# Optimization experiments

Measured on AMD Instinct MI355X. Metric: run time of the kernel, lower is better.

The kernel has to match this reference:

```python
import jax, jax.numpy as jnp
import numpy as np

B, C, H = 2, 32, 64  # batch, base channel, bottleneck spatial size
EPS = 1e-5


def _conv(x, w, b, pad):
    # standard NCHW conv, stride 1
    out = jax.lax.conv_general_dilated(x, w, (1, 1), [(pad, pad), (pad, pad)],
                                       dimension_numbers=("NCHW", "OIHW", "NCHW"))
    return out + b[None, :, None, None]


def _inorm(x):
    # InstanceNorm2d, affine=False (torch default)
    m = jnp.mean(x, axis=(2, 3), keepdims=True)
    v = jnp.var(x, axis=(2, 3), keepdims=True)
    return (x - m) * jax.lax.rsqrt(v + EPS)


def _patches3(x):
    # x: (B,C,H,W) -> (B,C,9,H-2,W-2); 3x3 patches, stride 1, VALID
    oh, ow = x.shape[-2] - 2, x.shape[-1] - 2
    return jnp.stack([x[:, :, i:i + oh, j:j + ow] for i in range(3) for j in range(3)], axis=2)


def _pac_kernel(g):
    # gaussian pixel-adaptive kernel (NVlabs/pac, kernel_type='gaussian', normalize_kernel=False)
    # g: (B,Cg,H,W) -> K: (B,9,H,W), K = exp(-0.5*||f_nbr - f_center||^2)
    gp = jnp.pad(g, ((0, 0), (0, 0), (1, 1), (1, 1)))
    p = _patches3(gp)                      # (B,Cg,9,H,W)
    d = p - g[:, :, None]                  # center is offset (1,1) == g itself
    return jnp.exp(-0.5 * jnp.sum(d * d, axis=1))


def _pacconvT(x, g, w, b):
    # PacConvTranspose2d: kernel_size=3, stride=2, padding=1, output_padding=1
    # native impl: zero-upsample, pad (k-1)-p=1 left/top and 1+out_pad=2 right/bottom,
    # then pixel-adaptive conv with weight.permute(1,0,2,3) (no spatial flip, per PAC).
    Bc, Cin, Hh, Ww = x.shape
    z = jnp.zeros((Bc, Cin, 2 * Hh - 1, 2 * Ww - 1), x.dtype).at[:, :, ::2, ::2].set(x)
    z = jnp.pad(z, ((0, 0), (0, 0), (1, 2), (1, 2)))
    p = _patches3(z)                       # (B,Cin,9,2H,2W)
    k = _pac_kernel(g)                     # (B,9,2H,2W)
    wf = jnp.transpose(w, (1, 0, 2, 3)).reshape(w.shape[1], w.shape[0], 9)  # (Cout,Cin,9)
    out = jnp.einsum('bckhw,bkhw,ock->bohw', p, k, wf)
    return out + b[None, :, None, None]


def _w(key, shape, scale):
    return jax.random.normal(key, shape, dtype=jnp.float32) * scale


def setup_inputs():
    key = jax.random.key(0)
    ks = jax.random.split(key, 20)
    return {
        "x": jax.random.normal(ks[0], (B, 8 * C, H, H), jnp.float32),
        "ef_lv2": jax.random.normal(ks[1], (B, 2 * C, 2 * H, 2 * H), jnp.float32),
        "ef_lv1": jax.random.normal(ks[2], (B, C, 4 * H, 4 * H), jnp.float32),
        "W_down": _w(ks[3], (4 * C, 8 * C, 3, 3), (8 * C * 9) ** -0.5),
        "b_down": _w(ks[4], (4 * C,), 0.01),
        "W_mid": _w(ks[5], (4 * C, 4 * C, 1, 1), (4 * C) ** -0.5),
        "b_mid": _w(ks[6], (4 * C,), 0.01),
        "W_adj2": _w(ks[7], (4 * C, 2 * C, 3, 3), 0.002),  # small: keeps gaussian kernel non-degenerate
        "b_adj2": _w(ks[8], (4 * C,), 0.01),
        "W_adj1": _w(ks[9], (2 * C, C, 3, 3), 0.004),
        "b_adj1": _w(ks[10], (2 * C,), 0.01),
        "W16": _w(ks[11], (4 * C, 2 * C, 3, 3), (4 * C * 9) ** -0.5),  # convT layout (Cin,Cout,kh,kw)
        "b16": _w(ks[12], (2 * C,), 0.01),
        "W20": _w(ks[13], (2 * C, C, 3, 3), (2 * C * 9) ** -0.5),
        "b20": _w(ks[14], (C,), 0.01),
        "W24": _w(ks[15], (3, C, 3, 3), (C * 9) ** -0.5),
        "b24": _w(ks[16], (3,), 0.01),
    }


def reference(x, ef_lv2, ef_lv1, W_down, b_down, W_mid, b_mid, W_adj2, b_adj2,
              W_adj1, b_adj1, W16, b16, W20, b20, W24, b24):
    x = _conv(_inorm(x), W_down, b_down, 1)          # layer13: norm + channel-down 8C->4C
    x = _conv(x, W_mid, b_mid, 0) + x                # middle_layer13 1x1 + residual
    g2 = _conv(ef_lv2, W_adj2, b_adj2, 1)            # adjust_ef_lv2 2C->4C
    x = _pacconvT(x, g2, W16, b16)                   # layer16: 4C->2C, x2 spatial
    x = _inorm(x) + x                                # layer17 + residual (twice)
    x = _inorm(x) + x
    g1 = _conv(ef_lv1, W_adj1, b_adj1, 1)            # adjust_ef_lv1 C->2C
    x = _pacconvT(x, g1, W20, b20)                   # layer20: 2C->C, x2 spatial
    x = _inorm(x) + x                                # layer21 + residual (twice)
    x = _inorm(x) + x
    return _conv(x, W24, b24, 1)                     # layer24: C->3
```

## Files before the change

### kernel.cpp

```cpp
#include <hip/hip_runtime.h>

#define EPS 1e-5f

typedef short sh8 __attribute__((ext_vector_type(8)));
typedef float f32x4 __attribute__((ext_vector_type(4)));

__device__ __forceinline__ ushort f2b(float f) {
    unsigned u = __float_as_uint(f);
    u += 0x7fffu + ((u >> 16) & 1u);
    return (ushort)(u >> 16);
}

__device__ __forceinline__ void istat_body(int ch, const float* __restrict__ in,
                                           float* st, int HW)
{
    __shared__ double sh[512];
    const float* p = in + (size_t)ch * HW;
    double s = 0.0, s2 = 0.0;
    for (int i = threadIdx.x * 4; i < HW; i += 1024) {
        float4 v = *(const float4*)(p + i);
        s  += (double)v.x + (double)v.y + (double)v.z + (double)v.w;
        s2 += (double)v.x * v.x + (double)v.y * v.y
            + (double)v.z * v.z + (double)v.w * v.w;
    }
    sh[threadIdx.x] = s; sh[256 + threadIdx.x] = s2;
    __syncthreads();
    for (int o = 128; o > 0; o >>= 1) {
        if ((int)threadIdx.x < o) {
            sh[threadIdx.x]       += sh[threadIdx.x + o];
            sh[256 + threadIdx.x] += sh[256 + threadIdx.x + o];
        }
        __syncthreads();
    }
    if (threadIdx.x == 0) {
        double m = sh[0] / (double)HW;
        double v = sh[256] / (double)HW - m * m;
        st[2 * ch]     = (float)m;
        st[2 * ch + 1] = (float)(v < 0.0 ? 0.0 : v);
    }
}

__device__ __forceinline__ void ipad_body(int bxi, int b,
    const float* __restrict__ in, const float* __restrict__ st,
    ushort* __restrict__ ob, int C, int H, int W, int pad, int n4)
{
    int idx = bxi * 256 + threadIdx.x;
    if (idx >= n4) return;
    int cpp = C >> 2;
    int pp = idx / cpp, c0 = (idx - pp * cpp) * 4;
    int Wp = W + 2 * pad, Hp = H + 2 * pad;
    int yp = pp / Wp, xp = pp - yp * Wp;
    int y = yp - pad, x = xp - pad;
    ushort4 o;
    if (y >= 0 && y < H && x >= 0 && x < W) {
        size_t HW = (size_t)H * W;
        const float* ib = in + (size_t)b * C * HW + (size_t)y * W + x;
        #pragma unroll
        for (int u = 0; u < 4; u++) {
            int chg = b * C + c0 + u;
            float m = st[2 * chg];
            float inv = rsqrtf(st[2 * chg + 1] + EPS);
            float v = ib[(size_t)(c0 + u) * HW];
            ((ushort*)&o)[u] = f2b((v - m) * inv);
        }
    } else { o.x = o.y = o.z = o.w = 0; }
    *(ushort4*)(ob + ((size_t)b * Hp * Wp + pp) * C + c0) = o;
}

__device__ __forceinline__ void pad_body(int bxi, int b,
    const float* __restrict__ in, ushort* __restrict__ ob,
    int C, int H, int W, int pad, int n4)
{
    int idx = bxi * 256 + threadIdx.x;
    if (idx >= n4) return;
    int cpp = C >> 2;
    int pp = idx / cpp, c0 = (idx - pp * cpp) * 4;
    int Wp = W + 2 * pad, Hp = H + 2 * pad;
    int yp = pp / Wp, xp = pp - yp * Wp;
    int y = yp - pad, x = xp - pad;
    ushort4 o;
    if (y >= 0 && y < H && x >= 0 && x < W) {
        const float* ib = in + ((size_t)b * C) * H * W + (size_t)y * W + x;
        size_t HW = (size_t)H * W;
        o.x = f2b(ib[(size_t)(c0    ) * HW]);
        o.y = f2b(ib[(size_t)(c0 + 1) * HW]);
        o.z = f2b(ib[(size_t)(c0 + 2) * HW]);
        o.w = f2b(ib[(size_t)(c0 + 3) * HW]);
    } else { o.x = o.y = o.z = o.w = 0; }
    *(ushort4*)(ob + ((size_t)b * Hp * Wp + pp) * C + c0) = o;
}

__device__ __forceinline__ void wprep_body(int bxi,
    const float* W16, const float* W20, const float* Wd, const float* Wa2,
    const float* Wa1,
    ushort* wT1b, ushort* wT2b, ushort* wbD, ushort* wbA2b, ushort* wbA1b)
{
    int idx = bxi * 256 + threadIdx.x;
    if (idx < 73728) {
        int to = idx / 128, ci = idx - to * 128;
        int t = to / 64, o = to - t * 64;
        wT1b[idx] = f2b(W16[((size_t)ci * 64 + o) * 9 + t]);
        return;
    } idx -= 73728;
    if (idx < 18432) {
        int to = idx / 64, ci = idx - to * 64;
        int t = to / 32, o = to - t * 32;
        wT2b[idx] = f2b(W20[((size_t)ci * 32 + o) * 9 + t]);
        return;
    } idx -= 18432;
    if (idx < 294912) {
        int co = idx / 2304, r = idx - co * 2304;
        int t = r / 256, ci = r - t * 256;
        wbD[idx] = f2b(Wd[((size_t)co * 256 + ci) * 9 + t]);
        return;
    } idx -= 294912;
    if (idx < 73728) {
        int co = idx / 576, r = idx - co * 576;
        int t = r / 64, ci = r - t * 64;
        wbA2b[idx] = f2b(Wa2[((size_t)co * 64 + ci) * 9 + t]);
        return;
    } idx -= 73728;
    if (idx < 18432) {
        int co = idx / 288, r = idx - co * 288;
        int t = r / 32, ci = r - t * 32;
        wbA1b[idx] = f2b(Wa1[((size_t)co * 32 + ci) * 9 + t]);
        return;
    }
}

template<int CI, int TAPS, int KCH, int CPB>
__device__ __forceinline__ void mg2f_body(int bx, int by, int b,
    const ushort* __restrict__ inb, const ushort* __restrict__ wb,
    const float* __restrict__ bias, float* __restrict__ outp,
    int wshift, int Wp, size_t in_bstride, size_t out_bstride, int HW,
    ushort* bsm)
{
    constexpr int CPBSH = (CPB == 1) ? 0 : (CPB == 2) ? 1 : 2;
    constexpr int SPR   = TAPS * CPB;
    constexpr int TOT   = TAPS * KCH;
    constexpr int PS    = SPR * 32 + 8;

    int tid = threadIdx.x;
    int wv = tid >> 6, l = tid & 63;
    int lane16 = l & 15, quad = l >> 4;
    int klane = quad * 8;
    int pb = bx * 128 + wv * 32;
    int nb0 = by * 32;

    int base[2];
    #pragma unroll
    for (int i = 0; i < 2; i++) {
        int pm = pb + i * 16 + lane16;
        if (TAPS == 9) {
            int W = 1 << wshift;
            int y = pm >> wshift, xx = pm & (W - 1);
            base[i] = (y + 1) * Wp + (xx + 1);
        } else base[i] = pm;
    }
    int nn[2];
    nn[0] = nb0 + lane16; nn[1] = nb0 + 16 + lane16;

    const ushort* inbb = inb + (size_t)b * in_bstride + klane;
    const ushort* bp0 = bsm + lane16 * PS + klane;
    const ushort* bp1 = bsm + (16 + lane16) * PS + klane;

    f32x4 vz = {0.f, 0.f, 0.f, 0.f};
    f32x4 acc[2][2] = {{vz, vz}, {vz, vz}};
    sh8 A[3][2];

    #define LDA(ss, av) { \
        int r_ = (ss) / SPR; int l_ = (ss) - r_ * SPR; \
        int t_ = l_ >> CPBSH; int ch_ = r_ * CPB + (l_ & (CPB - 1)); \
        int dof_ = 0; \
        if (TAPS == 9) { \
            int dy_ = (t_ * 43) >> 7; \
            int dx_ = t_ - dy_ * 3; \
            dof_ = (dy_ - 1) * Wp + (dx_ - 1); \
        } \
        av[0] = *(const sh8*)(inbb + (size_t)(base[0] + dof_) * CI + (ch_ << 5)); \
        av[1] = *(const sh8*)(inbb + (size_t)(base[1] + dof_) * CI + (ch_ << 5)); \
    }

    LDA(0, A[0])
    if (TOT > 1) LDA(1, A[1])

    #pragma unroll
    for (int r = 0; r < KCH / CPB; r++) {
        if (r) __syncthreads();
        {
            constexpr int elems = 32 * SPR * 4;
            for (int j = tid; j < elems; j += 256) {
                int n  = j / (SPR * 4);
                int rr = j - n * (SPR * 4);
                int kc = rr >> 2, c8 = rr & 3;
                int t_ = kc >> CPBSH, co = kc & (CPB - 1);
                int ch_ = r * CPB + co;
                sh8 v = *(const sh8*)(wb
                    + ((size_t)(nb0 + n) * TAPS + t_) * CI + (ch_ << 5) + (c8 << 3));
                *(sh8*)(bsm + n * PS + (kc << 5) + (c8 << 3)) = v;
            }
        }
        __syncthreads();
        #pragma unroll
        for (int li = 0; li < SPR; li++) {
            const int s = r * SPR + li;
            if (s + 2 < TOT) LDA(s + 2, A[(s + 2) % 3])
            sh8 b0 = *(const sh8*)(bp0 + (li << 5));
            sh8 b1 = *(const sh8*)(bp1 + (li << 5));
            acc[0][0] = __builtin_amdgcn_mfma_f32_16x16x32_bf16(A[s % 3][0], b0, acc[0][0], 0, 0, 0);
            acc[0][1] = __builtin_amdgcn_mfma_f32_16x16x32_bf16(A[s % 3][0], b1, acc[0][1], 0, 0, 0);
            acc[1][0] = __builtin_amdgcn_mfma_f32_16x16x32_bf16(A[s % 3][1], b0, acc[1][0], 0, 0, 0);
            acc[1][1] = __builtin_amdgcn_mfma_f32_16x16x32_bf16(A[s % 3][1], b1, acc[1][1], 0, 0, 0);
        }
    }
    #undef LDA

    float* ob = outp + (size_t)b * out_bstride;
    #pragma unroll
    for (int j = 0; j < 2; j++) {
        float bb = bias ? bias[nn[j]] : 0.f;
        #pragma unroll
        for (int i = 0; i < 2; i++) {
            int p0 = pb + i * 16 + quad * 4;
            *(float4*)(ob + (size_t)nn[j] * HW + p0) =
                make_float4(acc[i][j][0] + bb, acc[i][j][1] + bb,
                            acc[i][j][2] + bb, acc[i][j][3] + bb);
        }
    }
}

__device__ __forceinline__ void pack4_body(int bxi, int zy,
    const float* __restrict__ g, float* __restrict__ part,
    int Cg, int CS, int H, int W, int NS, size_t SS)
{
    int b = zy / NS, sl = zy - b * NS;
    int WC = W >> 2;
    int idx = bxi * 256 + threadIdx.x;
    int y = idx / WC, xc = idx - y * WC;
    int x0 = xc << 2;
    bool lz = (x0 == 0), rz = (x0 + 4 == W);
    float acc[9][4];
    #pragma unroll
    for (int t = 0; t < 9; t++)
        #pragma unroll
        for (int p = 0; p < 4; p++) acc[t][p] = 0.f;

    const float* gb = g + ((size_t)b * Cg + sl * CS) * H * W;
    for (int ci = 0; ci < CS; ci++) {
        const float* gc = gb + (size_t)ci * H * W;
        float e[3][6];
        #pragma unroll
        for (int r = 0; r < 3; r++) {
            int yy = y + r - 1;
            float4 v = make_float4(0.f, 0.f, 0.f, 0.f);
            if (yy >= 0 && yy < H)
                v = *(const float4*)(gc + (size_t)yy * W + x0);
            float lf = __shfl_up(v.w, 1);
            float rt = __shfl_down(v.x, 1);
            e[r][0] = lz ? 0.f : lf;
            e[r][1] = v.x; e[r][2] = v.y; e[r][3] = v.z; e[r][4] = v.w;
            e[r][5] = rz ? 0.f : rt;
        }
        #pragma unroll
        for (int i = 0; i < 3; i++)
            #pragma unroll
            for (int j = 0; j < 3; j++)
                #pragma unroll
                for (int p = 0; p < 4; p++) {
                    float d = e[i][p + j] - e[1][p + 1];
                    acc[i * 3 + j][p] = fmaf(d, d, acc[i * 3 + j][p]);
                }
    }
    size_t HW = (size_t)H * W;
    #pragma unroll
    for (int t = 0; t < 9; t++) {
        float4 o;
        if (NS == 1) {
            o = make_float4(expf(-0.5f * acc[t][0]), expf(-0.5f * acc[t][1]),
                            expf(-0.5f * acc[t][2]), expf(-0.5f * acc[t][3]));
        } else {
            o = make_float4(acc[t][0], acc[t][1], acc[t][2], acc[t][3]);
        }
        *(float4*)(part + (size_t)sl * SS + ((size_t)b * 9 + t) * HW
                   + (size_t)y * W + x0) = o;
    }
}

__device__ __forceinline__ void reduce_body(int bxi,
    const float* __restrict__ part, const float* __restrict__ bias,
    const float* res, float* out, int HW, int Co, int NS, size_t SS)
{
    int i4 = (bxi * 256 + threadIdx.x) * 4;
    float4 a = make_float4(0.f, 0.f, 0.f, 0.f);
    for (int s = 0; s < NS; s++) {
        float4 p = *(const float4*)(part + (size_t)s * SS + i4);
        a.x += p.x; a.y += p.y; a.z += p.z; a.w += p.w;
    }
    int c = (i4 / HW) % Co;
    float bb = bias[c];
    if (res) {
        float4 r = *(const float4*)(res + i4);
        a.x += r.x; a.y += r.y; a.z += r.z; a.w += r.w;
    }
    *(float4*)(out + i4) = make_float4(a.x + bb, a.y + bb, a.z + bb, a.w + bb);
}

__device__ __forceinline__ void expcomb_body(int bxi,
    const float* __restrict__ part, float* __restrict__ K, int NS, size_t SS)
{
    int i4 = (bxi * 256 + threadIdx.x) * 4;
    float4 a = make_float4(0.f, 0.f, 0.f, 0.f);
    for (int s = 0; s < NS; s++) {
        float4 p = *(const float4*)(part + (size_t)s * SS + i4);
        a.x += p.x; a.y += p.y; a.z += p.z; a.w += p.w;
    }
    *(float4*)(K + i4) = make_float4(expf(-0.5f * a.x), expf(-0.5f * a.y),
                                     expf(-0.5f * a.z), expf(-0.5f * a.w));
}

template<int NCO>
__device__ __forceinline__ void conv1x1_body(int bx, int by, int bz,
    const float* __restrict__ in, const float* __restrict__ w,
    float* __restrict__ outp, int C, int CS, int HW, int NS, size_t SS)
{
    int b = bz / NS, sl = bz - b * NS;
    int x0 = (bx * 256 + threadIdx.x) * 4;
    int co0 = by * NCO;
    float acc[NCO][4];
    #pragma unroll
    for (int j = 0; j < NCO; j++)
        #pragma unroll
        for (int p = 0; p < 4; p++) acc[j][p] = 0.f;
    const float* ib = in + ((size_t)b * C + sl * CS) * HW;
    for (int ci = 0; ci < CS; ci++) {
        float4 v = *(const float4*)(ib + (size_t)ci * HW + x0);
        int cig = sl * CS + ci;
        #pragma unroll
        for (int j = 0; j < NCO; j++) {
            float wv = w[(size_t)(co0 + j) * C + cig];
            acc[j][0] = fmaf(v.x, wv, acc[j][0]);
            acc[j][1] = fmaf(v.y, wv, acc[j][1]);
            acc[j][2] = fmaf(v.z, wv, acc[j][2]);
            acc[j][3] = fmaf(v.w, wv, acc[j][3]);
        }
    }
    #pragma unroll
    for (int j = 0; j < NCO; j++) {
        float* op = outp + (size_t)sl * SS + ((size_t)b * C + co0 + j) * HW + x0;
        *(float4*)op = make_float4(acc[j][0], acc[j][1], acc[j][2], acc[j][3]);
    }
}

__global__ __launch_bounds__(256) void pro_k(
    const float* x, const float* ef2, const float* ef1,
    const float* W16, const float* W20, const float* Wd, const float* Wa2,
    const float* Wa1,
    ushort* wT1b, ushort* wT2b, ushort* wbD, ushort* wbA2b, ushort* wbA1b,
    float* st0, ushort* padA2b, ushort* padA1b)
{
    int bid = blockIdx.x;
    if (bid < 1872) {
        wprep_body(bid, W16, W20, Wd, Wa2, Wa1, wT1b, wT2b, wbD, wbA2b, wbA1b);
        return;
    } bid -= 1872;
    if (bid < 512) { istat_body(bid, x, st0, 4096); return; } bid -= 512;
    if (bid < 2114) {
        pad_body(bid % 1057, bid / 1057, ef2, padA2b, 64, 128, 128, 1, 270400);
        return;
    } bid -= 2114;
    pad_body(bid % 2081, bid / 2081, ef1, padA1b, 32, 256, 256, 1, 532512);
}

__global__ __launch_bounds__(256) void l1_k(
    const float* x, const float* st0, ushort* padDb,
    const ushort* padA2b, const ushort* wbA2b, const float* ba2, float* g2,
    const ushort* padA1b, const ushort* wbA1b, const float* ba1, float* g1)
{
    __shared__ ushort smem[32 * (9 * 32 + 8)];
    int bid = blockIdx.x;
    if (bid < 2178) {
        ipad_body(bid % 1089, bid / 1089, x, st0, padDb, 256, 64, 64, 1, 278784);
        return;
    } bid -= 2178;
    if (bid < 1024) {
        mg2f_body<64, 9, 2, 1>(bid & 127, (bid >> 7) & 3, bid >> 9,
            padA2b, wbA2b, ba2, g2, 7, 130,
            (size_t)1081600, (size_t)2097152, 16384, smem);
        return;
    } bid -= 1024;
    mg2f_body<32, 9, 1, 1>(bid & 511, (bid >> 9) & 1, bid >> 10,
        padA1b, wbA1b, ba1, g1, 8, 258,
        (size_t)2130048, (size_t)4194304, 65536, smem);
}

__global__ __launch_bounds__(256) void l2_k(
    const ushort* padDb, const ushort* wbD, const float* bd, float* x1,
    const float* g1, float* K1, const float* g2, float* PK2)
{
    __shared__ ushort smem[32 * (9 * 32 + 8)];
    int bid = blockIdx.x;
    if (bid < 256) {
        mg2f_body<256, 9, 8, 1>(bid & 31, (bid >> 5) & 3, bid >> 7,
            padDb, wbD, bd, x1, 6, 66,
            (size_t)1115136, (size_t)524288, 4096, smem);
        return;
    } bid -= 256;
    if (bid < 128) {
        pack4_body(bid & 63, bid >> 6, g1, K1, 64, 64, 256, 256, 1, (size_t)0);
        return;
    } bid -= 128;
    pack4_body(bid & 15, bid >> 4, g2, PK2, 128, 64, 128, 128, 2, (size_t)294912);
}

__global__ __launch_bounds__(256) void l3_k(
    const float* x1, const float* Wm, float* Pm,
    const float* PK2, float* K2)
{
    int bid = blockIdx.x;
    if (bid < 512) {
        conv1x1_body<8>(bid & 3, (bid >> 2) & 15, bid >> 6,
                        x1, Wm, Pm, 128, 32, 4096, 4, (size_t)1048576);
        return;
    }
    expcomb_body(bid - 512, PK2, K2, 2, (size_t)294912);
}

__global__ __launch_bounds__(256) void istat1_k(const float* __restrict__ in,
                                                float* st, int HW)
{
    istat_body(blockIdx.x, in, st, HW);
}

template<int CI, int TAPS, int KCH, int CPB>
__global__ __launch_bounds__(256) void mg2f_k(
    const ushort* __restrict__ inb, const ushort* __restrict__ wb,
    const float* __restrict__ bias, float* __restrict__ outp,
    int wshift, int Wp, size_t in_bstride, size_t out_bstride, int HW)
{
    constexpr int PS = TAPS * CPB * 32 + 8;
    __shared__ ushort smem[32 * PS];
    mg2f_body<CI, TAPS, KCH, CPB>(blockIdx.x, blockIdx.y, blockIdx.z,
        inb, wb, bias, outp, wshift, Wp, in_bstride, out_bstride, HW, smem);
}

__global__ __launch_bounds__(256) void iapad_k(const float* __restrict__ in,
    const float* __restrict__ st, ushort* __restrict__ ob, int HW, int Co)
{
    int i4 = (blockIdx.x * 256 + threadIdx.x) * 4;
    int ch = i4 / HW;
    int p = i4 - ch * HW;
    int b = ch / Co, c = ch - b * Co;
    float m = st[2 * ch];
    float inv = rsqrtf(st[2 * ch + 1] + EPS);
    float4 v = *(const float4*)(in + i4);
    ushort* op = ob + ((size_t)b * HW + p) * Co + c;
    op[0]              = f2b(v.x + 2.f * (v.x - m) * inv);
    op[(size_t)Co]     = f2b(v.y + 2.f * (v.y - m) * inv);
    op[(size_t)Co * 2] = f2b(v.z + 2.f * (v.z - m) * inv);
    op[(size_t)Co * 3] = f2b(v.w + 2.f * (v.w - m) * inv);
}

template<int NCO>
__global__ __launch_bounds__(256) void conv3x3_d(const float* __restrict__ in,
    const float* __restrict__ w, const float* __restrict__ bias,
    float* __restrict__ outp, const float* __restrict__ st,
    int Ci, int CS, int H, int W, int Co, int NS, size_t SS)
{
    int z = blockIdx.z;
    int b = z / NS, sl = z - b * NS;
    int WC = W >> 2;
    int idx = blockIdx.x * 256 + threadIdx.x;
    int xc = idx % WC, y = idx / WC;
    int x0 = xc << 2;
    bool lz = (x0 == 0), rz = (x0 + 4 == W);
    int co0 = blockIdx.y * NCO;
    float acc[NCO][4];
    #pragma unroll
    for (int j = 0; j < NCO; j++)
        #pragma unroll
        for (int p = 0; p < 4; p++) acc[j][p] = 0.f;

    const float* ib = in + ((size_t)b * Ci + sl * CS) * H * W;
    for (int ci = 0; ci < CS; ci++) {
        const float* ic = ib + (size_t)ci * H * W;
        int cig = sl * CS + ci;
        float sa = 1.f, sb = 0.f;
        if (st) {
            int chg = b * Ci + cig;
            float m = st[2 * chg];
            float inv = rsqrtf(st[2 * chg + 1] + EPS);
            sa = 1.f + 2.f * inv;
            sb = -2.f * m * inv;
        }
        float e[3][6];
        #pragma unroll
        for (int r = 0; r < 3; r++) {
            int yy = y + r - 1;
            float4 v = make_float4(0.f, 0.f, 0.f, 0.f);
            if (yy >= 0 && yy < H) {
                v = *(const float4*)(ic + (size_t)yy * W + x0);
                if (st) {
                    v.x = fmaf(v.x, sa, sb); v.y = fmaf(v.y, sa, sb);
                    v.z = fmaf(v.z, sa, sb); v.w = fmaf(v.w, sa, sb);
                }
            }
            float lf = __shfl_up(v.w, 1);
            float rt = __shfl_down(v.x, 1);
            e[r][0] = lz ? 0.f : lf;
            e[r][1] = v.x; e[r][2] = v.y; e[r][3] = v.z; e[r][4] = v.w;
            e[r][5] = rz ? 0.f : rt;
        }
        #pragma unroll
        for (int j = 0; j < NCO; j++) {
            const float* wj = w + ((size_t)(co0 + j) * Ci + cig) * 9;
            #pragma unroll
            for (int r = 0; r < 3; r++) {
                float w0 = wj[3 * r], w1 = wj[3 * r + 1], w2 = wj[3 * r + 2];
                #pragma unroll
                for (int p = 0; p < 4; p++)
                    acc[j][p] = fmaf(e[r][p], w0,
                                fmaf(e[r][p + 1], w1,
                                fmaf(e[r][p + 2], w2, acc[j][p])));
            }
        }
    }
    size_t HW = (size_t)H * W;
    #pragma unroll
    for (int j = 0; j < NCO; j++) {
        float bb = bias ? bias[co0 + j] : 0.f;
        float4 o = make_float4(acc[j][0] + bb, acc[j][1] + bb,
                               acc[j][2] + bb, acc[j][3] + bb);
        float* op = outp + (size_t)sl * SS
                  + ((size_t)b * Co + co0 + j) * HW + (size_t)y * W + x0;
        *(float4*)op = o;
    }
}

__global__ __launch_bounds__(256) void reduce_k(const float* __restrict__ part,
    const float* __restrict__ bias, const float* res, float* out,
    int HW, int Co, int NS, size_t SS)
{
    reduce_body(blockIdx.x, part, bias, res, out, HW, Co, NS, SS);
}

__global__ __launch_bounds__(256) void reduceb_k(const float* __restrict__ part,
    const float* __restrict__ bias, const float* __restrict__ res,
    ushort* __restrict__ ob, int HW, int Co, int NS, size_t SS)
{
    int i4 = (blockIdx.x * 256 + threadIdx.x) * 4;
    int ch = i4 / HW;
    int p = i4 - ch * HW;
    int b = ch / Co, c = ch - b * Co;
    float4 a = make_float4(0.f, 0.f, 0.f, 0.f);
    for (int s = 0; s < NS; s++) {
        float4 pv = *(const float4*)(part + (size_t)s * SS + i4);
        a.x += pv.x; a.y += pv.y; a.z += pv.z; a.w += pv.w;
    }
    float bb = bias[c];
    float4 r = *(const float4*)(res + i4);
    a.x += r.x + bb; a.y += r.y + bb; a.z += r.z + bb; a.w += r.w + bb;
    ushort* op = ob + ((size_t)b * HW + p) * Co + c;
    op[0]              = f2b(a.x);
    op[(size_t)Co]     = f2b(a.y);
    op[(size_t)Co * 2] = f2b(a.z);
    op[(size_t)Co * 3] = f2b(a.w);
}

template<int NCO>
__global__ __launch_bounds__(256) void pacsc_k(const float* __restrict__ Gin,
    const float* __restrict__ K, const float* __restrict__ bias,
    float* __restrict__ out, int Cout, int Hi, int Wi, size_t gstride)
{
    int b = blockIdx.z;
    int H = Hi << 1, W = Wi << 1;
    int HW = H * W, HWi = Hi * Wi, WC = W >> 2;
    int idx = blockIdx.x * 256 + threadIdx.x;
    int half = (H >> 1) * WC;
    int py = (idx >= half) ? 1 : 0;
    int r = idx - py * half;
    int ry = r / WC;
    int y = 2 * ry + py;
    int x0 = (r - ry * WC) << 2;
    int yi = y >> 1, xi0 = x0 >> 1;
    int co0 = blockIdx.y * NCO;
    const float* G  = Gin + (size_t)b * gstride;
    const float* Kb = K + (size_t)b * 9 * HW;
    float* ob = out + (size_t)b * Cout * HW;
    size_t krow = (size_t)y * W + x0;
    bool vok = (xi0 + 2 < Wi);

    if (py == 0) {
        float k4a = Kb[(size_t)4 * HW + krow],     k4b = Kb[(size_t)4 * HW + krow + 2];
        float k3a = Kb[(size_t)3 * HW + krow + 1], k3b = Kb[(size_t)3 * HW + krow + 3];
        float k5a = Kb[(size_t)5 * HW + krow + 1], k5b = Kb[(size_t)5 * HW + krow + 3];
        #pragma unroll
        for (int j = 0; j < NCO; j++) {
            int co = co0 + j;
            size_t rowb = (size_t)yi * Wi + xi0;
            const float* g3 = G + (size_t)(3 * Cout + co) * HWi + rowb;
            const float* g4 = G + (size_t)(4 * Cout + co) * HWi + rowb;
            const float* g5 = G + (size_t)(5 * Cout + co) * HWi + rowb;
            float bb = bias[co];
            float g5b = vok ? g5[2] : 0.f;
            float o0 = fmaf(k4a, g4[0], bb);
            float o1 = fmaf(k3a, g3[0], fmaf(k5a, g5[1], bb));
            float o2 = fmaf(k4b, g4[1], bb);
            float o3 = fmaf(k3b, g3[1], fmaf(k5b, g5b, bb));
            *(float4*)(ob + (size_t)co * HW + krow) = make_float4(o0, o1, o2, o3);
        }
    } else {
        bool yok = (yi + 1 < Hi);
        float k1a = Kb[(size_t)1 * HW + krow],     k1b = Kb[(size_t)1 * HW + krow + 2];
        float k7a = Kb[(size_t)7 * HW + krow],     k7b = Kb[(size_t)7 * HW + krow + 2];
        float k0a = Kb[(size_t)0 * HW + krow + 1], k0b = Kb[(size_t)0 * HW + krow + 3];
        float k2a = Kb[(size_t)2 * HW + krow + 1], k2b = Kb[(size_t)2 * HW + krow + 3];
        float k6a = Kb[(size_t)6 * HW + krow + 1], k6b = Kb[(size_t)6 * HW + krow + 3];
        float k8a = Kb[(size_t)8 * HW + krow + 1], k8b = Kb[(size_t)8 * HW + krow + 3];
        #pragma unroll
        for (int j = 0; j < NCO; j++) {
            int co = co0 + j;
            size_t row0 = (size_t)yi * Wi + xi0;
            size_t row1 = (size_t)(yi + 1) * Wi + xi0;
            const float* g0 = G + (size_t)(0 * Cout + co) * HWi + row0;
            const float* g1 = G + (size_t)(1 * Cout + co) * HWi + row0;
            const float* g2 = G + (size_t)(2 * Cout + co) * HWi + row0;
            const float* g6 = G + (size_t)(6 * Cout + co) * HWi + row1;
            const float* g7 = G + (size_t)(7 * Cout + co) * HWi + row1;
            const float* g8 = G + (size_t)(8 * Cout + co) * HWi + row1;
            float bb = bias[co];
            float g2b = vok ? g2[2] : 0.f;
            float g6a = yok ? g6[0] : 0.f, g6b = yok ? g6[1] : 0.f;
            float g7a = yok ? g7[0] : 0.f, g7b = yok ? g7[1] : 0.f;
            float g8a = yok ? g8[1] : 0.f;
            float g8b = (yok && vok) ? g8[2] : 0.f;
            float o0 = fmaf(k1a, g1[0], fmaf(k7a, g7a, bb));
            float o1 = fmaf(k0a, g0[0], fmaf(k2a, g2[1],
                       fmaf(k6a, g6a, fmaf(k8a, g8a, bb))));
            float o2 = fmaf(k1b, g1[1], fmaf(k7b, g7b, bb));
            float o3 = fmaf(k0b, g0[1], fmaf(k2b, g2b,
                       fmaf(k6b, g6b, fmaf(k8b, g8b, bb))));
            *(float4*)(ob + (size_t)co * HW + krow) = make_float4(o0, o1, o2, o3);
        }
    }
}

extern "C" void kernel_launch(void* const* d_in, const int* in_sizes, int n_in,
                              void* d_out, int out_size, void* d_ws, size_t ws_size,
                              hipStream_t stream)
{
    const float* x   = (const float*)d_in[0];
    const float* ef2 = (const float*)d_in[1];
    const float* ef1 = (const float*)d_in[2];
    const float* Wd  = (const float*)d_in[3];
    const float* bd  = (const float*)d_in[4];
    const float* Wm  = (const float*)d_in[5];
    const float* bm  = (const float*)d_in[6];
    const float* Wa2 = (const float*)d_in[7];
    const float* ba2 = (const float*)d_in[8];
    const float* Wa1 = (const float*)d_in[9];
    const float* ba1 = (const float*)d_in[10];
    const float* W16 = (const float*)d_in[11];
    const float* b16 = (const float*)d_in[12];
    const float* W20 = (const float*)d_in[13];
    const float* b20 = (const float*)d_in[14];
    const float* W24 = (const float*)d_in[15];
    const float* b24 = (const float*)d_in[16];
    float* out = (float*)d_out;

    float* P = (float*)d_ws;
    size_t o = 0;
    auto take = [&](size_t n) { float* p = P + o; o += n; return p; };
    ushort* padDb  = (ushort*)take(1115136);
    ushort* wbD    = (ushort*)take(147456);
    float*  x1     = take(1048576);
    float*  Pm     = take(4194304);
    ushort* x2b    = (ushort*)take(524288);
    ushort* padA2b = (ushort*)take(1081600);
    ushort* wbA2b  = (ushort*)take(36864);
    float*  g2     = take(4194304);
    float*  PK2    = take(589824);
    float*  K2     = take(294912);
    float*  Gin1   = take(4718592);
    float*  x3     = take(2097152);
    ushort* x3b    = (ushort*)take(1048576);
    ushort* padA1b = (ushort*)take(2130048);
    ushort* wbA1b  = (ushort*)take(9216);
    float*  g1     = take(4194304);
    float*  K1     = take(1179648);
    float*  Gin2   = take(9437184);
    float*  x5     = take(4194304);
    float*  Pf     = take(1572864);
    ushort* wT1b   = (ushort*)take(36864);
    ushort* wT2b   = (ushort*)take(9216);
    float*  ST     = take(1408);
    float* st0 = ST; float* st3 = ST + 1024; float* st5 = ST + 1280;

    pro_k<<<dim3(8660), dim3(256), 0, stream>>>(
        x, ef2, ef1, W16, W20, Wd, Wa2, Wa1,
        wT1b, wT2b, wbD, wbA2b, wbA1b, st0, padA2b, padA1b);

    l1_k<<<dim3(5250), dim3(256), 0, stream>>>(
        x, st0, padDb, padA2b, wbA2b, ba2, g2, padA1b, wbA1b, ba1, g1);

    l2_k<<<dim3(448), dim3(256), 0, stream>>>(
        padDb, wbD, bd, x1, g1, K1, g2, PK2);

    l3_k<<<dim3(800), dim3(256), 0, stream>>>(x1, Wm, Pm, PK2, K2);

    reduceb_k<<<dim3(1024), dim3(256), 0, stream>>>(Pm, bm, x1, x2b, 4096, 128, 4, 1048576);

    mg2f_k<128, 1, 4, 4><<<dim3(32, 18, 2), dim3(256), 0, stream>>>(
        x2b, wT1b, nullptr, Gin1, 0, 0,
        (size_t)524288, (size_t)2359296, 4096);
    pacsc_k<2><<<dim3(16, 32, 2), dim3(256), 0, stream>>>(
        Gin1, K2, b16, x3, 64, 64, 64, (size_t)2359296);

    istat1_k<<<dim3(128), dim3(256), 0, stream>>>(x3, st3, 16384);
    iapad_k<<<dim3(2048), dim3(256), 0, stream>>>(x3, st3, x3b, 16384, 64);

    mg2f_k<64, 1, 2, 2><<<dim3(128, 9, 2), dim3(256), 0, stream>>>(
        x3b, wT2b, nullptr, Gin2, 0, 0,
        (size_t)1048576, (size_t)4718592, 16384);
    pacsc_k<2><<<dim3(64, 16, 2), dim3(256), 0, stream>>>(
        Gin2, K1, b20, x5, 32, 128, 128, (size_t)4718592);

    istat1_k<<<dim3(64), dim3(256), 0, stream>>>(x5, st5, 65536);

    conv3x3_d<3><<<dim3(64, 1, 8), dim3(256), 0, stream>>>(
        x5, W24, nullptr, Pf, st5, 32, 8, 256, 256, 3, 4, (size_t)393216);
    reduce_k<<<dim3(384), dim3(256), 0, stream>>>(Pf, b24, nullptr, out, 65536, 3, 4, 393216);
}
```

Before: 370.0 us.

## Split-K the down conv across 8 slices and fuse 1x1 conv with residual

The 3x3 channel-down MFMA conv (256 input channels) is split into 8 input-channel slices, each writing partial sums. A reduce then adds bias to form x1, raising the block count from 256 to 2048 for better occupancy. The 1x1 middle conv now runs in one kernel with weights in shared memory and fuses bias, residual and the bf16 channel-last packing, replacing the separate split conv plus reduceb pass. The g2 pack step also computes K2 in a single slice, which drops the expcomb step. The cost is a larger partial buffer and extra memory traffic for the split-K reduction.

```diff
diff --git a/kernel.cpp b/kernel.cpp
--- a/kernel.cpp
+++ b/kernel.cpp
@@ -129,17 +129,19 @@
 }
 
 template<int CI, int TAPS, int KCH, int CPB>
-__device__ __forceinline__ void mg2f_body(int bx, int by, int b,
+__device__ __forceinline__ void mg2f_body(int bx, int by, int bz,
     const ushort* __restrict__ inb, const ushort* __restrict__ wb,
     const float* __restrict__ bias, float* __restrict__ outp,
-    int wshift, int Wp, size_t in_bstride, size_t out_bstride, int HW,
-    ushort* bsm)
+    int wshift, int Wp, int NS, size_t SS,
+    size_t in_bstride, size_t out_bstride, int HW, ushort* bsm)
 {
     constexpr int CPBSH = (CPB == 1) ? 0 : (CPB == 2) ? 1 : 2;
     constexpr int SPR   = TAPS * CPB;
     constexpr int TOT   = TAPS * KCH;
     constexpr int PS    = SPR * 32 + 8;
 
+    int b = bz / NS, sl = bz - b * NS;
+    int cilo = sl * (KCH * 32);
     int tid = threadIdx.x;
     int wv = tid >> 6, l = tid & 63;
     int lane16 = l & 15, quad = l >> 4;
@@ -160,7 +162,8 @@
     int nn[2];
     nn[0] = nb0 + lane16; nn[1] = nb0 + 16 + lane16;
 
-    const ushort* inbb = inb + (size_t)b * in_bstride + klane;
+    const ushort* inbb = inb + (size_t)b * in_bstride + cilo + klane;
+    const ushort* wbs  = wb + cilo;
     const ushort* bp0 = bsm + lane16 * PS + klane;
     const ushort* bp1 = bsm + (16 + lane16) * PS + klane;
 
@@ -195,7 +198,7 @@
                 int kc = rr >> 2, c8 = rr & 3;
                 int t_ = kc >> CPBSH, co = kc & (CPB - 1);
                 int ch_ = r * CPB + co;
-                sh8 v = *(const sh8*)(wb
+                sh8 v = *(const sh8*)(wbs
                     + ((size_t)(nb0 + n) * TAPS + t_) * CI + (ch_ << 5) + (c8 << 3));
                 *(sh8*)(bsm + n * PS + (kc << 5) + (c8 << 3)) = v;
             }
@@ -215,7 +218,7 @@
     }
     #undef LDA
 
-    float* ob = outp + (size_t)b * out_bstride;
+    float* ob = outp + (size_t)sl * SS + (size_t)b * out_bstride;
     #pragma unroll
     for (int j = 0; j < 2; j++) {
         float bb = bias ? bias[nn[j]] : 0.f;
@@ -305,52 +308,6 @@
     *(float4*)(out + i4) = make_float4(a.x + bb, a.y + bb, a.z + bb, a.w + bb);
 }
 
-__device__ __forceinline__ void expcomb_body(int bxi,
-    const float* __restrict__ part, float* __restrict__ K, int NS, size_t SS)
-{
-    int i4 = (bxi * 256 + threadIdx.x) * 4;
-    float4 a = make_float4(0.f, 0.f, 0.f, 0.f);
-    for (int s = 0; s < NS; s++) {
-        float4 p = *(const float4*)(part + (size_t)s * SS + i4);
-        a.x += p.x; a.y += p.y; a.z += p.z; a.w += p.w;
-    }
-    *(float4*)(K + i4) = make_float4(expf(-0.5f * a.x), expf(-0.5f * a.y),
-                                     expf(-0.5f * a.z), expf(-0.5f * a.w));
-}
-
-template<int NCO>
-__device__ __forceinline__ void conv1x1_body(int bx, int by, int bz,
-    const float* __restrict__ in, const float* __restrict__ w,
-    float* __restrict__ outp, int C, int CS, int HW, int NS, size_t SS)
-{
-    int b = bz / NS, sl = bz - b * NS;
-    int x0 = (bx * 256 + threadIdx.x) * 4;
-    int co0 = by * NCO;
-    float acc[NCO][4];
-    #pragma unroll
-    for (int j = 0; j < NCO; j++)
-        #pragma unroll
-        for (int p = 0; p < 4; p++) acc[j][p] = 0.f;
-    const float* ib = in + ((size_t)b * C + sl * CS) * HW;
-    for (int ci = 0; ci < CS; ci++) {
-        float4 v = *(const float4*)(ib + (size_t)ci * HW + x0);
-        int cig = sl * CS + ci;
-        #pragma unroll
-        for (int j = 0; j < NCO; j++) {
-            float wv = w[(size_t)(co0 + j) * C + cig];
-            acc[j][0] = fmaf(v.x, wv, acc[j][0]);
-            acc[j][1] = fmaf(v.y, wv, acc[j][1]);
-            acc[j][2] = fmaf(v.z, wv, acc[j][2]);
-            acc[j][3] = fmaf(v.w, wv, acc[j][3]);
-        }
-    }
-    #pragma unroll
-    for (int j = 0; j < NCO; j++) {
-        float* op = outp + (size_t)sl * SS + ((size_t)b * C + co0 + j) * HW + x0;
-        *(float4*)op = make_float4(acc[j][0], acc[j][1], acc[j][2], acc[j][3]);
-    }
-}
-
 __global__ __launch_bounds__(256) void pro_k(
     const float* x, const float* ef2, const float* ef1,
     const float* W16, const float* W20, const float* Wd, const float* Wa2,
@@ -384,45 +341,82 @@
     } bid -= 2178;
     if (bid < 1024) {
         mg2f_body<64, 9, 2, 1>(bid & 127, (bid >> 7) & 3, bid >> 9,
-            padA2b, wbA2b, ba2, g2, 7, 130,
+            padA2b, wbA2b, ba2, g2, 7, 130, 1, (size_t)0,
             (size_t)1081600, (size_t)2097152, 16384, smem);
         return;
     } bid -= 1024;
     mg2f_body<32, 9, 1, 1>(bid & 511, (bid >> 9) & 1, bid >> 10,
-        padA1b, wbA1b, ba1, g1, 8, 258,
+        padA1b, wbA1b, ba1, g1, 8, 258, 1, (size_t)0,
         (size_t)2130048, (size_t)4194304, 65536, smem);
 }
 
 __global__ __launch_bounds__(256) void l2_k(
-    const ushort* padDb, const ushort* wbD, const float* bd, float* x1,
-    const float* g1, float* K1, const float* g2, float* PK2)
+    const ushort* padDb, const ushort* wbD, float* Pd,
+    const float* g1, float* K1, const float* g2, float* K2)
 {
     __shared__ ushort smem[32 * (9 * 32 + 8)];
     int bid = blockIdx.x;
-    if (bid < 256) {
-        mg2f_body<256, 9, 8, 1>(bid & 31, (bid >> 5) & 3, bid >> 7,
-            padDb, wbD, bd, x1, 6, 66,
+    if (bid < 2048) {
+        mg2f_body<256, 9, 1, 1>(bid & 31, (bid >> 5) & 3, bid >> 7,
+            padDb, wbD, nullptr, Pd, 6, 66, 8, (size_t)1048576,
             (size_t)1115136, (size_t)524288, 4096, smem);
         return;
-    } bid -= 256;
+    } bid -= 2048;
     if (bid < 128) {
         pack4_body(bid & 63, bid >> 6, g1, K1, 64, 64, 256, 256, 1, (size_t)0);
         return;
     } bid -= 128;
-    pack4_body(bid & 15, bid >> 4, g2, PK2, 128, 64, 128, 128, 2, (size_t)294912);
-}
-
-__global__ __launch_bounds__(256) void l3_k(
-    const float* x1, const float* Wm, float* Pm,
-    const float* PK2, float* K2)
-{
-    int bid = blockIdx.x;
-    if (bid < 512) {
-        conv1x1_body<8>(bid & 3, (bid >> 2) & 15, bid >> 6,
-                        x1, Wm, Pm, 128, 32, 4096, 4, (size_t)1048576);
-        return;
-    }
-    expcomb_body(bid - 512, PK2, K2, 2, (size_t)294912);
+    pack4_body(bid & 15, bid >> 4, g2, K2, 128, 128, 128, 128, 1, (size_t)0);
+}
+
+__global__ __launch_bounds__(256) void conv1x1f_k(
+    const float* __restrict__ x1, const float* __restrict__ Wm,
+    const float* __restrict__ bm, ushort* __restrict__ x2b)
+{
+    __shared__ float wsm[1024];
+    int b = blockIdx.z;
+    int co0 = blockIdx.y * 8;
+    int tid = threadIdx.x;
+    for (int j = tid; j < 1024; j += 256) {
+        int co = j >> 7, ci = j & 127;
+        wsm[j] = Wm[(size_t)(co0 + co) * 128 + ci];
+    }
+    __syncthreads();
+    int px0 = (blockIdx.x * 256 + tid) * 4;
+    const float* ib = x1 + (size_t)b * 524288 + px0;
+    float acc[8][4];
+    #pragma unroll
+    for (int j = 0; j < 8; j++)
+        #pragma unroll
+        for (int p = 0; p < 4; p++) acc[j][p] = 0.f;
+    for (int ci = 0; ci < 128; ci++) {
+        float4 v = *(const float4*)(ib + (size_t)ci * 4096);
+        #pragma unroll
+        for (int j = 0; j < 8; j++) {
+            float wv = wsm[j * 128 + ci];
+            acc[j][0] = fmaf(v.x, wv, acc[j][0]);
+            acc[j][1] = fmaf(v.y, wv, acc[j][1]);
+            acc[j][2] = fmaf(v.z, wv, acc[j][2]);
+            acc[j][3] = fmaf(v.w, wv, acc[j][3]);
+        }
+    }
+    float vals[4][8];
+    #pragma unroll
+    for (int j = 0; j < 8; j++) {
+        float4 r = *(const float4*)(ib + (size_t)(co0 + j) * 4096);
+        float bb = bm[co0 + j];
+        vals[0][j] = acc[j][0] + r.x + bb;
+        vals[1][j] = acc[j][1] + r.y + bb;
+        vals[2][j] = acc[j][2] + r.z + bb;
+        vals[3][j] = acc[j][3] + r.w + bb;
+    }
+    #pragma unroll
+    for (int p = 0; p < 4; p++) {
+        sh8 ov;
+        #pragma unroll
+        for (int j = 0; j < 8; j++) ((ushort*)&ov)[j] = f2b(vals[p][j]);
+        *(sh8*)(x2b + ((size_t)b * 4096 + px0 + p) * 128 + co0) = ov;
+    }
 }
 
 __global__ __launch_bounds__(256) void istat1_k(const float* __restrict__ in,
@@ -435,12 +429,13 @@
 __global__ __launch_bounds__(256) void mg2f_k(
     const ushort* __restrict__ inb, const ushort* __restrict__ wb,
     const float* __restrict__ bias, float* __restrict__ outp,
-    int wshift, int Wp, size_t in_bstride, size_t out_bstride, int HW)
+    int wshift, int Wp, int NS, size_t SS,
+    size_t in_bstride, size_t out_bstride, int HW)
 {
     constexpr int PS = TAPS * CPB * 32 + 8;
     __shared__ ushort smem[32 * PS];
     mg2f_body<CI, TAPS, KCH, CPB>(blockIdx.x, blockIdx.y, blockIdx.z,
-        inb, wb, bias, outp, wshift, Wp, in_bstride, out_bstride, HW, smem);
+        inb, wb, bias, outp, wshift, Wp, NS, SS, in_bstride, out_bstride, HW, smem);
 }
 
 __global__ __launch_bounds__(256) void iapad_k(const float* __restrict__ in,
@@ -541,29 +536,6 @@
     int HW, int Co, int NS, size_t SS)
 {
     reduce_body(blockIdx.x, part, bias, res, out, HW, Co, NS, SS);
-}
-
-__global__ __launch_bounds__(256) void reduceb_k(const float* __restrict__ part,
-    const float* __restrict__ bias, const float* __restrict__ res,
-    ushort* __restrict__ ob, int HW, int Co, int NS, size_t SS)
-{
-    int i4 = (blockIdx.x * 256 + threadIdx.x) * 4;
-    int ch = i4 / HW;
-    int p = i4 - ch * HW;
-    int b = ch / Co, c = ch - b * Co;
-    float4 a = make_float4(0.f, 0.f, 0.f, 0.f);
-    for (int s = 0; s < NS; s++) {
-        float4 pv = *(const float4*)(part + (size_t)s * SS + i4);
-        a.x += pv.x; a.y += pv.y; a.z += pv.z; a.w += pv.w;
-    }
-    float bb = bias[c];
-    float4 r = *(const float4*)(res + i4);
-    a.x += r.x + bb; a.y += r.y + bb; a.z += r.z + bb; a.w += r.w + bb;
-    ushort* op = ob + ((size_t)b * HW + p) * Co + c;
-    op[0]              = f2b(a.x);
-    op[(size_t)Co]     = f2b(a.y);
-    op[(size_t)Co * 2] = f2b(a.z);
-    op[(size_t)Co * 3] = f2b(a.w);
 }
 
 template<int NCO>
@@ -672,13 +644,12 @@
     auto take = [&](size_t n) { float* p = P + o; o += n; return p; };
     ushort* padDb  = (ushort*)take(1115136);
     ushort* wbD    = (ushort*)take(147456);
+    float*  Pd     = take(8388608);
     float*  x1     = take(1048576);
-    float*  Pm     = take(4194304);
     ushort* x2b    = (ushort*)take(524288);
     ushort* padA2b = (ushort*)take(1081600);
     ushort* wbA2b  = (ushort*)take(36864);
     float*  g2     = take(4194304);
-    float*  PK2    = take(589824);
     float*  K2     = take(294912);
     float*  Gin1   = take(4718592);
     float*  x3     = take(2097152);
@@ -702,15 +673,15 @@
     l1_k<<<dim3(5250), dim3(256), 0, stream>>>(
         x, st0, padDb, padA2b, wbA2b, ba2, g2, padA1b, wbA1b, ba1, g1);
 
-    l2_k<<<dim3(448), dim3(256), 0, stream>>>(
-        padDb, wbD, bd, x1, g1, K1, g2, PK2);
-
-    l3_k<<<dim3(800), dim3(256), 0, stream>>>(x1, Wm, Pm, PK2, K2);
-
-    reduceb_k<<<dim3(1024), dim3(256), 0, stream>>>(Pm, bm, x1, x2b, 4096, 128, 4, 1048576);
+    l2_k<<<dim3(2208), dim3(256), 0, stream>>>(
+        padDb, wbD, Pd, g1, K1, g2, K2);
+
+    reduce_k<<<dim3(1024), dim3(256), 0, stream>>>(Pd, bd, nullptr, x1, 4096, 128, 8, 1048576);
+
+    conv1x1f_k<<<dim3(4, 16, 2), dim3(256), 0, stream>>>(x1, Wm, bm, x2b);
 
     mg2f_k<128, 1, 4, 4><<<dim3(32, 18, 2), dim3(256), 0, stream>>>(
-        x2b, wT1b, nullptr, Gin1, 0, 0,
+        x2b, wT1b, nullptr, Gin1, 0, 0, 1, (size_t)0,
         (size_t)524288, (size_t)2359296, 4096);
     pacsc_k<2><<<dim3(16, 32, 2), dim3(256), 0, stream>>>(
         Gin1, K2, b16, x3, 64, 64, 64, (size_t)2359296);
@@ -719,7 +690,7 @@
     iapad_k<<<dim3(2048), dim3(256), 0, stream>>>(x3, st3, x3b, 16384, 64);
 
     mg2f_k<64, 1, 2, 2><<<dim3(128, 9, 2), dim3(256), 0, stream>>>(
-        x3b, wT2b, nullptr, Gin2, 0, 0,
+        x3b, wT2b, nullptr, Gin2, 0, 0, 1, (size_t)0,
         (size_t)1048576, (size_t)4718592, 16384);
     pacsc_k<2><<<dim3(64, 16, 2), dim3(256), 0, stream>>>(
         Gin2, K1, b20, x5, 32, 128, 128, (size_t)4718592);
```

Measured after the change: 435.8 us. 17.8% more time.
